# Kernel tuning notes

Hardware: AMD Instinct MI355X
Metric: run time of the kernel (lower is better)

Reference implementation:

```python
import jax, jax.numpy as jnp
import numpy as np

VOCAB = 4  # token alphabet size used in setup_inputs


def setup_inputs() -> dict:
    key = jax.random.key(0)
    k1, k2 = jax.random.split(key)
    xq = jax.random.randint(k1, (8192, 512), 0, VOCAB, dtype=jnp.int32)
    xp = jax.random.randint(k2, (8192, 512), 0, VOCAB, dtype=jnp.int32)
    return {"xq": xq, "xp": xp}


def reference(xq, xp):
    # Pairwise Hamming distance: dists[n, m] = sum_d [xq[n, d] != xp[m, d]].
    # Expressed as D minus the match count, computed as a one-hot GEMM
    # (matches[n,m] = sum_{d,v} 1[xq[n,d]==v] * 1[xp[m,d]==v]) so the whole
    # NxMxD reduction is a single fused contraction instead of the original
    # per-row broadcast-compare loop. Exact in fp32 since counts <= D = 512.
    D = xq.shape[1]
    qh = jax.nn.one_hot(xq, VOCAB, dtype=jnp.float32)  # [N, D, V]
    ph = jax.nn.one_hot(xp, VOCAB, dtype=jnp.float32)  # [M, D, V]
    matches = jnp.einsum('ndv,mdv->nm', qh, ph)        # [N, M]
    return (jnp.float32(D) - matches).astype(jnp.int32)
```

## Files before the change

kernel.cpp:

```cpp
#include <hip/hip_runtime.h>
#include <stdint.h>


#define NROWS 8192

typedef int   v4i  __attribute__((ext_vector_type(4)));
typedef int   v8i  __attribute__((ext_vector_type(8)));
typedef float v16f __attribute__((ext_vector_type(16)));

__global__ __launch_bounds__(512) void pack_kernel(
    const int* __restrict__ xq, const int* __restrict__ xp,
    uint8_t* __restrict__ qpk, uint8_t* __restrict__ ppk) {
  __shared__ uint8_t lt[64 * 384];
  const int bid = blockIdx.x;
  const int op  = bid & 1;
  const int dh  = (bid >> 1) & 1;
  const int R64 = bid >> 2;
  const int t   = threadIdx.x;
  const int* src = op ? xp : xq;
  uint8_t*   dst = op ? ppk : qpk;
  const int row0 = R64 * 64;
  const int d0   = dh * 256;

  #pragma unroll
  for (int i = 0; i < 8; ++i) {
    const int idx = i * 512 + t;
    const int rl = idx >> 6, q = idx & 63;
    const int4 a = ((const int4*)(src + (size_t)(row0 + rl) * 512 + d0))[q];
    const int tok[4] = {a.x, a.y, a.z, a.w};
    uint32_t n0 = 0, n1 = 0, n2 = 0;
    #pragma unroll
    for (int j = 0; j < 4; ++j) {
      const uint32_t b1 = (tok[j] >> 1) & 1, b0 = tok[j] & 1;
      n0 |= (0x2u | (b1 << 3)) << (4 * j);
      n1 |= (0x2u | (b0 << 3)) << (4 * j);
      n2 |= (0x2u | ((b1 ^ b0) << 3)) << (4 * j);
    }
    uint8_t* p = lt + rl * 384 + (((q >> 3) ^ (rl & 7)) << 4) + (q & 7) * 2;
    *(uint16_t*)(p)       = (uint16_t)n0;
    *(uint16_t*)(p + 128) = (uint16_t)n1;
    *(uint16_t*)(p + 256) = (uint16_t)n2;
  }
  __syncthreads();

  const size_t Rg = R64 >> 2;
  const int rb = (R64 & 3) * 64;
  #pragma unroll
  for (int i = 0; i < 3; ++i) {
    const int o = i * 512 + t;
    const int c = o >> 9, sg = (o >> 6) & 7, rl = o & 63;
    const int kt = c * 2 + dh;
    const uint4 v = *(const uint4*)(lt + rl * 384 + c * 128 + ((sg ^ (rl & 7)) << 4));
    *(uint4*)(dst + (((Rg * 6 + kt) * 8 + sg) * 256 + rb + rl) * 16) = v;
  }
}

__global__ __launch_bounds__(256, 2) void hamming_mfma(
    const uint8_t* __restrict__ Apk, const uint8_t* __restrict__ Bpk,
    int* __restrict__ out) {
  const int t = threadIdx.x, l = t & 63, w = t >> 6;
  const int wr = w >> 1, wc = w & 1;

  const int bid = blockIdx.x;
  const int nid = (bid & 7) * 256 + (bid >> 3);
  const int q = nid & 63, p = nid >> 6;
  const int br = (p >> 3) * 8 + (q >> 3);
  const int bc = (p & 7) * 8 + (q & 7);

  const int g = l >> 5, ll = l & 31;
  const uint8_t* abase = Apk + (size_t)br * 196608 + g * 4096
                       + (size_t)(wr * 128 + ll) * 16;
  const uint8_t* bbase = Bpk + (size_t)(bc >> 1) * 196608 + g * 4096
                       + (size_t)((bc & 1) * 128 + wc * 64 + ll) * 16;

  v4i af[4][4], bf[4][2];
  v16f acc[4][2] = {};

  #pragma unroll
  for (int i = 0; i < 4; ++i) {
    #pragma unroll
    for (int m = 0; m < 4; ++m)
      af[i][m] = *(const v4i*)(abase + i * 8192 + m * 512);
    #pragma unroll
    for (int n = 0; n < 2; ++n)
      bf[i][n] = *(const v4i*)(bbase + i * 8192 + n * 512);
  }

  for (int so = 0; so < 24; so += 4) {
    const int snext = (so + 4 == 24) ? 0 : so + 4;
    const uint8_t* pa = abase + snext * 8192;
    const uint8_t* pb = bbase + snext * 8192;
    #pragma unroll
    for (int i = 0; i < 4; ++i) {
      #pragma unroll
      for (int m = 0; m < 4; ++m)
        #pragma unroll
        for (int n = 0; n < 2; ++n) {
          const v8i av = (v8i){af[i][m][0], af[i][m][1], af[i][m][2], af[i][m][3],
                               0, 0, 0, 0};
          const v8i bv = (v8i){bf[i][n][0], bf[i][n][1], bf[i][n][2], bf[i][n][3],
                               0, 0, 0, 0};
          acc[m][n] = __builtin_amdgcn_mfma_scale_f32_32x32x64_f8f6f4(
              av, bv, acc[m][n], 4 , 4 ,
              0, 0x7F7F7F7F, 0, 0x7F7F7F7F);
        }
      #pragma unroll
      for (int m = 0; m < 4; ++m)
        af[i][m] = *(const v4i*)(pa + i * 8192 + m * 512);
      #pragma unroll
      for (int n = 0; n < 2; ++n)
        bf[i][n] = *(const v4i*)(pb + i * 8192 + n * 512);
    }
  }

  const int rbase = br * 256 + wr * 128 + 4 * (l >> 5);
  const int cbase = bc * 128 + wc * 64 + (l & 31);
  #pragma unroll
  for (int m = 0; m < 4; ++m)
    #pragma unroll
    for (int n = 0; n < 2; ++n) {
      const int col = cbase + n * 32;
      #pragma unroll
      for (int reg = 0; reg < 16; ++reg) {
        const int orow = rbase + m * 32 + (reg & 3) + 8 * (reg >> 2);
        __builtin_nontemporal_store(
            512 - (((int)acc[m][n][reg] + 512) >> 2),
            &out[(size_t)orow * NROWS + col]);
      }
    }
}

extern "C" void kernel_launch(void* const* d_in, const int* in_sizes, int n_in,
                              void* d_out, int out_size, void* d_ws, size_t ws_size,
                              hipStream_t stream) {
  const int* xq = (const int*)d_in[0];
  const int* xp = (const int*)d_in[1];
  int* out = (int*)d_out;

  uint8_t* qpk = (uint8_t*)d_ws;
  uint8_t* ppk = qpk + (size_t)NROWS * 768;

  pack_kernel<<<512, 512, 0, stream>>>(xq, xp, qpk, ppk);
  hamming_mfma<<<2048, 256, 0, stream>>>(qpk, ppk, out);
}
```

Baseline: 342.1 us.

## Stage operand tiles through LDS with triple-buffered direct global-to-LDS loads

Replaces direct per-wave register prefetch of packed operands with a triple-buffered LDS pipeline filled by global_load_lds, shared across the four waves of a block. The output tile shrinks from 256x128 to 128x128 with the grid doubled, occupancy is raised to 3 blocks per CU, and MFMA sections get raised priority. Output stores switch from nontemporal to regular stores. This removes redundant global loads of shared A/B fragments across waves, at the cost of block-wide barriers and smaller per-wave tiles with less register reuse.

```diff
diff --git a/kernel.cpp b/kernel.cpp
--- a/kernel.cpp
+++ b/kernel.cpp
@@ -7,6 +7,9 @@
 typedef int   v4i  __attribute__((ext_vector_type(4)));
 typedef int   v8i  __attribute__((ext_vector_type(8)));
 typedef float v16f __attribute__((ext_vector_type(16)));
+
+#define AS1(p) ((const __attribute__((address_space(1))) void*)(p))
+#define AS3(p) ((__attribute__((address_space(3))) void*)(p))
 
 __global__ __launch_bounds__(512) void pack_kernel(
     const int* __restrict__ xq, const int* __restrict__ xp,
@@ -55,77 +58,97 @@
   }
 }
 
-__global__ __launch_bounds__(256, 2) void hamming_mfma(
+__global__ __launch_bounds__(256, 3) void hamming_mfma(
     const uint8_t* __restrict__ Apk, const uint8_t* __restrict__ Bpk,
     int* __restrict__ out) {
+  __shared__ __align__(128) uint8_t lds[49152];
+
   const int t = threadIdx.x, l = t & 63, w = t >> 6;
   const int wr = w >> 1, wc = w & 1;
+  const int g = l >> 5, ll = l & 31;
 
   const int bid = blockIdx.x;
-  const int nid = (bid & 7) * 256 + (bid >> 3);
-  const int q = nid & 63, p = nid >> 6;
-  const int br = (p >> 3) * 8 + (q >> 3);
-  const int bc = (p & 7) * 8 + (q & 7);
+  const int nid = (bid & 7) * 512 + (bid >> 3);
+  const int pch = nid >> 6, q = nid & 63;
+  const int br = (pch >> 3) * 8 + (q >> 3);
+  const int bc = (pch & 7) * 8 + (q & 7);
 
-  const int g = l >> 5, ll = l & 31;
-  const uint8_t* abase = Apk + (size_t)br * 196608 + g * 4096
-                       + (size_t)(wr * 128 + ll) * 16;
-  const uint8_t* bbase = Bpk + (size_t)(bc >> 1) * 196608 + g * 4096
-                       + (size_t)((bc & 1) * 128 + wc * 64 + ll) * 16;
+  const int g2 = t >> 7, j = t & 127;
+  const uint8_t* srcA = Apk + (size_t)(br >> 1) * 196608 + g2 * 4096
+                      + ((br & 1) * 128 + j) * 16;
+  const uint8_t* srcB = Bpk + (size_t)(bc >> 1) * 196608 + g2 * 4096
+                      + ((bc & 1) * 128 + j) * 16;
 
-  v4i af[4][4], bf[4][2];
-  v16f acc[4][2] = {};
+  #define STAGE(c, buf) do {                                                   \
+    __builtin_amdgcn_global_load_lds(AS1(srcA + (2*(c))   * 8192),             \
+        AS3(lds + (buf) * 16384 +  0   + t * 16), 16, 0, 0);                   \
+    __builtin_amdgcn_global_load_lds(AS1(srcA + (2*(c)+1) * 8192),             \
+        AS3(lds + (buf) * 16384 + 4096 + t * 16), 16, 0, 0);                   \
+    __builtin_amdgcn_global_load_lds(AS1(srcB + (2*(c))   * 8192),             \
+        AS3(lds + (buf) * 16384 + 8192 + t * 16), 16, 0, 0);                   \
+    __builtin_amdgcn_global_load_lds(AS1(srcB + (2*(c)+1) * 8192),             \
+        AS3(lds + (buf) * 16384 + 12288 + t * 16), 16, 0, 0);                  \
+  } while (0)
+
+  v16f acc[2][2] = {};
+
+  STAGE(0, 0);
+  STAGE(1, 1);
+
+  const int aoff = g * 2048 + (wr * 64 + ll) * 16;
+  const int boff = 8192 + g * 2048 + (wc * 64 + ll) * 16;
 
   #pragma unroll
-  for (int i = 0; i < 4; ++i) {
+  for (int c = 0; c < 12; ++c) {
+    const int buf = c % 3;
+    if (c == 11) asm volatile("s_waitcnt vmcnt(0)" ::: "memory");
+    else         asm volatile("s_waitcnt vmcnt(4)" ::: "memory");
+    __builtin_amdgcn_s_barrier();
+    if (c < 10) STAGE(c + 2, (c + 2) % 3);
+
+    const uint8_t* La = lds + buf * 16384;
+    v4i af[2][2], bf[2][2];
     #pragma unroll
-    for (int m = 0; m < 4; ++m)
-      af[i][m] = *(const v4i*)(abase + i * 8192 + m * 512);
+    for (int pp = 0; pp < 2; ++pp) {
+      #pragma unroll
+      for (int m = 0; m < 2; ++m)
+        af[pp][m] = *(const v4i*)(La + pp * 4096 + aoff + m * 512);
+      #pragma unroll
+      for (int n = 0; n < 2; ++n)
+        bf[pp][n] = *(const v4i*)(La + pp * 4096 + boff + n * 512);
+    }
+    asm volatile("s_waitcnt lgkmcnt(0)" ::: "memory");
+    __builtin_amdgcn_sched_barrier(0);
+    __builtin_amdgcn_s_setprio(1);
     #pragma unroll
-    for (int n = 0; n < 2; ++n)
-      bf[i][n] = *(const v4i*)(bbase + i * 8192 + n * 512);
-  }
-
-  for (int so = 0; so < 24; so += 4) {
-    const int snext = (so + 4 == 24) ? 0 : so + 4;
-    const uint8_t* pa = abase + snext * 8192;
-    const uint8_t* pb = bbase + snext * 8192;
-    #pragma unroll
-    for (int i = 0; i < 4; ++i) {
+    for (int pp = 0; pp < 2; ++pp)
       #pragma unroll
-      for (int m = 0; m < 4; ++m)
+      for (int m = 0; m < 2; ++m)
         #pragma unroll
         for (int n = 0; n < 2; ++n) {
-          const v8i av = (v8i){af[i][m][0], af[i][m][1], af[i][m][2], af[i][m][3],
-                               0, 0, 0, 0};
-          const v8i bv = (v8i){bf[i][n][0], bf[i][n][1], bf[i][n][2], bf[i][n][3],
-                               0, 0, 0, 0};
+          const v8i av = (v8i){af[pp][m][0], af[pp][m][1], af[pp][m][2],
+                               af[pp][m][3], 0, 0, 0, 0};
+          const v8i bv = (v8i){bf[pp][n][0], bf[pp][n][1], bf[pp][n][2],
+                               bf[pp][n][3], 0, 0, 0, 0};
           acc[m][n] = __builtin_amdgcn_mfma_scale_f32_32x32x64_f8f6f4(
               av, bv, acc[m][n], 4 , 4 ,
               0, 0x7F7F7F7F, 0, 0x7F7F7F7F);
         }
-      #pragma unroll
-      for (int m = 0; m < 4; ++m)
-        af[i][m] = *(const v4i*)(pa + i * 8192 + m * 512);
-      #pragma unroll
-      for (int n = 0; n < 2; ++n)
-        bf[i][n] = *(const v4i*)(pb + i * 8192 + n * 512);
-    }
+    __builtin_amdgcn_s_setprio(0);
+    __builtin_amdgcn_s_barrier();
   }
 
-  const int rbase = br * 256 + wr * 128 + 4 * (l >> 5);
-  const int cbase = bc * 128 + wc * 64 + (l & 31);
+  const int rbase = br * 128 + wr * 64 + 4 * g;
+  const int cbase = bc * 128 + wc * 64 + ll;
   #pragma unroll
-  for (int m = 0; m < 4; ++m)
+  for (int m = 0; m < 2; ++m)
     #pragma unroll
     for (int n = 0; n < 2; ++n) {
       const int col = cbase + n * 32;
       #pragma unroll
       for (int reg = 0; reg < 16; ++reg) {
         const int orow = rbase + m * 32 + (reg & 3) + 8 * (reg >> 2);
-        __builtin_nontemporal_store(
-            512 - (((int)acc[m][n][reg] + 512) >> 2),
-            &out[(size_t)orow * NROWS + col]);
+        out[(size_t)orow * NROWS + col] = 512 - (((int)acc[m][n][reg] + 512) >> 2);
       }
     }
 }
@@ -141,5 +164,5 @@
   uint8_t* ppk = qpk + (size_t)NROWS * 768;
 
   pack_kernel<<<512, 512, 0, stream>>>(xq, xp, qpk, ppk);
-  hamming_mfma<<<2048, 256, 0, stream>>>(qpk, ppk, out);
+  hamming_mfma<<<4096, 256, 0, stream>>>(qpk, ppk, out);
 }
```

After: 311.1 us. 9.0% less time.
